# Kernel tuning notes

Measured on AMD Instinct MI355X. Metric: run time of the kernel, lower is better.

Reference implementation:

```python
import jax, jax.numpy as jnp
import numpy as np

H = 512
NHALF = 32  # N // 2 complex conjugate pairs
LLEN = 8192


def setup_inputs() -> dict:
    key = jax.random.key(0)
    k1, k2, k3 = jax.random.split(key, 3)
    # log_dt ~ uniform in [log(dt_min), log(dt_max)]
    log_dt = jax.random.uniform(k1, (H,), dtype=jnp.float32) * (
        np.log(0.1) - np.log(0.001)) + np.log(0.001)
    # C: complex randn stored as (H, NHALF, 2) real view
    C = jax.random.normal(k2, (H, NHALF, 2), dtype=jnp.float32)
    log_A_real = jnp.log(0.5 * jnp.ones((H, NHALF), dtype=jnp.float32))
    A_imag = np.pi * jnp.broadcast_to(
        jnp.arange(NHALF, dtype=jnp.float32), (H, NHALF))
    return {"C": C, "log_dt": log_dt, "log_A_real": log_A_real,
            "A_imag": A_imag, "L": LLEN}


def reference(C, log_dt, log_A_real, A_imag, L):
    # zoh discretization of diagonal SSM -> kernel K of shape (H, L)
    dt = jnp.exp(log_dt)                                  # (H,)
    Cc = (C[..., 0] + 1j * C[..., 1]).astype(jnp.complex64)  # (H, n)
    A = (-jnp.exp(log_A_real) + 1j * A_imag).astype(jnp.complex64)  # (H, n)
    dtA = A * dt[:, None]                                 # (H, n)
    t = jnp.arange(L, dtype=jnp.float32)                  # (L,)
    C_scaled = Cc * (jnp.exp(dtA) - 1.0) / A              # (H, n)
    # Vandermonde: exp(dtA)^t over length L, reduce over n
    T = jnp.exp(dtA[:, :, None] * t[None, None, :])       # (H, n, L) complex
    K = 2.0 * jnp.einsum('hn,hnl->hl', C_scaled, T).real  # (H, L)
    return K
```

## Files before the change

kernel.cpp:

```cpp
#include <hip/hip_runtime.h>
#include <math.h>

#define HDIM  512
#define NH    32
#define LLEN  8192
#define BLOCK 256
#define CHUNK (LLEN / BLOCK)

__global__ __launch_bounds__(BLOCK) void s4d_kernel(
    const float* __restrict__ C,
    const float* __restrict__ log_dt,
    const float* __restrict__ log_A_real,
    const float* __restrict__ A_imag,
    float* __restrict__ out)
{
    __shared__ float  s_cre[NH], s_cim[NH];
    __shared__ float  s_wre[NH], s_wim[NH];
    __shared__ float  s_dre[NH];
    __shared__ double s_dim[NH];

    const int h   = blockIdx.x;
    const int tid = threadIdx.x;

    if (tid < NH) {
        const int n = tid;
        const double TWO_PI = 6.283185307179586476925287;
        const double dt  = exp((double)log_dt[h]);
        const double Are = -exp((double)log_A_real[h * NH + n]);
        const double Aim = (double)A_imag[h * NH + n];
        const double dre = Are * dt, dim = Aim * dt;

        double es, ec;
        sincos(dim, &es, &ec);
        const double em   = exp(dre);
        const double nre  = em * ec - 1.0, nim = em * es;
        const double den  = Are * Are + Aim * Aim;
        const double fre  = (nre * Are + nim * Aim) / den;
        const double fim  = (nim * Are - nre * Aim) / den;
        const double Cre  = (double)C[(h * NH + n) * 2 + 0];
        const double Cim  = (double)C[(h * NH + n) * 2 + 1];
        s_cre[n] = (float)(2.0 * (Cre * fre - Cim * fim));
        s_cim[n] = (float)(2.0 * (Cre * fim + Cim * fre));

        double r = dim * (double)BLOCK * (1.0 / TWO_PI);
        r -= floor(r);
        double ss, cc;
        sincos(r * TWO_PI, &ss, &cc);
        const double m = exp(dre * (double)BLOCK);
        s_wre[n] = (float)(m * cc);
        s_wim[n] = (float)(m * ss);
        s_dre[n] = (float)dre;
        s_dim[n] = dim;
    }
    __syncthreads();

    float acc[CHUNK];
#pragma unroll
    for (int j = 0; j < CHUNK; ++j) acc[j] = 0.0f;

    const float ftid = (float)tid;
#pragma unroll 1
    for (int n = 0; n < NH; ++n) {
        const float cr = s_cre[n], ci = s_cim[n];
        const float wr = s_wre[n], wi = s_wim[n];

        const double TWO_PI = 6.283185307179586476925287;
        double r = s_dim[n] * (double)tid * (1.0 / TWO_PI);
        r -= floor(r);
        float s, c;
        __sincosf((float)(r * TWO_PI), &s, &c);
        const float mag = __expf(s_dre[n] * ftid);
        float Tr = mag * c, Ti = mag * s;

#pragma unroll
        for (int j = 0; j < CHUNK; ++j) {
            acc[j] = fmaf(cr, Tr, fmaf(-ci, Ti, acc[j]));
            const float nTr = fmaf(Tr, wr, -Ti * wi);
            const float nTi = fmaf(Tr, wi,  Ti * wr);
            Tr = nTr; Ti = nTi;
        }
    }

    float* orow = out + (size_t)h * LLEN + tid;
#pragma unroll
    for (int j = 0; j < CHUNK; ++j) orow[j * BLOCK] = acc[j];
}

extern "C" void kernel_launch(void* const* d_in, const int* in_sizes, int n_in,
                              void* d_out, int out_size, void* d_ws, size_t ws_size,
                              hipStream_t stream) {
    const float* C          = (const float*)d_in[0];
    const float* log_dt     = (const float*)d_in[1];
    const float* log_A_real = (const float*)d_in[2];
    const float* A_imag     = (const float*)d_in[3];
    float* out = (float*)d_out;

    s4d_kernel<<<HDIM, BLOCK, 0, stream>>>(C, log_dt, log_A_real, A_imag, out);
}
```

Measured before the change: 88.33 us.

## Split L across two blocks per head and store float4 runs per thread

The grid becomes 2 blocks per head, each covering half of L, so 1024 blocks are launched instead of 512 and more of the GPU is occupied. Each thread now owns 4 consecutive positions per step: it builds them from a seed using the single-step rotation w1, then advances all four by a 1024-step rotation. This enables float4 vectorized stores. The cost is that the per-n setup (double-precision range reduction, sincos, exp) runs in twice as many blocks, and the length-3 recurrence chain adds a little float error.

```diff
diff --git a/kernel.cpp b/kernel.cpp
--- a/kernel.cpp
+++ b/kernel.cpp
@@ -1,11 +1,13 @@
 #include <hip/hip_runtime.h>
 #include <math.h>
 
-#define HDIM  512
-#define NH    32
-#define LLEN  8192
-#define BLOCK 256
-#define CHUNK (LLEN / BLOCK)
+#define HDIM   512
+#define NH     32
+#define LLEN   8192
+#define BLOCK  256
+#define LSPLIT 2
+#define LPB    (LLEN / LSPLIT)
+#define JSTEPS (LPB / (BLOCK * 4))
 
 __global__ __launch_bounds__(BLOCK) void s4d_kernel(
     const float* __restrict__ C,
@@ -15,11 +17,13 @@
     float* __restrict__ out)
 {
     __shared__ float  s_cre[NH], s_cim[NH];
-    __shared__ float  s_wre[NH], s_wim[NH];
+    __shared__ float  s_w1r[NH], s_w1i[NH];
+    __shared__ float  s_Wr[NH],  s_Wi[NH];
     __shared__ float  s_dre[NH];
     __shared__ double s_dim[NH];
 
-    const int h   = blockIdx.x;
+    const int h   = blockIdx.y;
+    const int ls  = blockIdx.x;
     const int tid = threadIdx.x;
 
     if (tid < NH) {
@@ -32,58 +36,85 @@
 
         double es, ec;
         sincos(dim, &es, &ec);
-        const double em   = exp(dre);
-        const double nre  = em * ec - 1.0, nim = em * es;
-        const double den  = Are * Are + Aim * Aim;
-        const double fre  = (nre * Are + nim * Aim) / den;
-        const double fim  = (nim * Are - nre * Aim) / den;
-        const double Cre  = (double)C[(h * NH + n) * 2 + 0];
-        const double Cim  = (double)C[(h * NH + n) * 2 + 1];
+        const double em  = exp(dre);
+        const double nre = em * ec - 1.0, nim = em * es;
+        const double den = Are * Are + Aim * Aim;
+        const double fre = (nre * Are + nim * Aim) / den;
+        const double fim = (nim * Are - nre * Aim) / den;
+        const double Cre = (double)C[(h * NH + n) * 2 + 0];
+        const double Cim = (double)C[(h * NH + n) * 2 + 1];
         s_cre[n] = (float)(2.0 * (Cre * fre - Cim * fim));
         s_cim[n] = (float)(2.0 * (Cre * fim + Cim * fre));
 
-        double r = dim * (double)BLOCK * (1.0 / TWO_PI);
+        s_w1r[n] = (float)(em * ec);
+        s_w1i[n] = (float)(em * es);
+
+        double r = dim * 1024.0 * (1.0 / TWO_PI);
         r -= floor(r);
         double ss, cc;
         sincos(r * TWO_PI, &ss, &cc);
-        const double m = exp(dre * (double)BLOCK);
-        s_wre[n] = (float)(m * cc);
-        s_wim[n] = (float)(m * ss);
+        const double m = exp(dre * 1024.0);
+        s_Wr[n] = (float)(m * cc);
+        s_Wi[n] = (float)(m * ss);
+
         s_dre[n] = (float)dre;
         s_dim[n] = dim;
     }
     __syncthreads();
 
-    float acc[CHUNK];
+    const int lbase = ls * LPB + 4 * tid;
+    const float flbase = (float)lbase;
+
+    float acc[JSTEPS][4];
 #pragma unroll
-    for (int j = 0; j < CHUNK; ++j) acc[j] = 0.0f;
+    for (int j = 0; j < JSTEPS; ++j)
+#pragma unroll
+        for (int k = 0; k < 4; ++k) acc[j][k] = 0.0f;
 
-    const float ftid = (float)tid;
 #pragma unroll 1
     for (int n = 0; n < NH; ++n) {
         const float cr = s_cre[n], ci = s_cim[n];
-        const float wr = s_wre[n], wi = s_wim[n];
+        const float w1r = s_w1r[n], w1i = s_w1i[n];
+        const float Wr = s_Wr[n],  Wi = s_Wi[n];
 
         const double TWO_PI = 6.283185307179586476925287;
-        double r = s_dim[n] * (double)tid * (1.0 / TWO_PI);
+        double r = s_dim[n] * (double)lbase * (1.0 / TWO_PI);
         r -= floor(r);
         float s, c;
         __sincosf((float)(r * TWO_PI), &s, &c);
-        const float mag = __expf(s_dre[n] * ftid);
-        float Tr = mag * c, Ti = mag * s;
+        const float mag = __expf(s_dre[n] * flbase);
+
+        float Tr[4], Ti[4];
+        Tr[0] = mag * c;
+        Ti[0] = mag * s;
+#pragma unroll
+        for (int k = 1; k < 4; ++k) {
+            Tr[k] = fmaf(Tr[k-1], w1r, -Ti[k-1] * w1i);
+            Ti[k] = fmaf(Tr[k-1], w1i,  Ti[k-1] * w1r);
+        }
 
 #pragma unroll
-        for (int j = 0; j < CHUNK; ++j) {
-            acc[j] = fmaf(cr, Tr, fmaf(-ci, Ti, acc[j]));
-            const float nTr = fmaf(Tr, wr, -Ti * wi);
-            const float nTi = fmaf(Tr, wi,  Ti * wr);
-            Tr = nTr; Ti = nTi;
+        for (int j = 0; j < JSTEPS; ++j) {
+#pragma unroll
+            for (int k = 0; k < 4; ++k)
+                acc[j][k] = fmaf(cr, Tr[k], fmaf(-ci, Ti[k], acc[j][k]));
+            if (j < JSTEPS - 1) {
+#pragma unroll
+                for (int k = 0; k < 4; ++k) {
+                    const float nTr = fmaf(Tr[k], Wr, -Ti[k] * Wi);
+                    const float nTi = fmaf(Tr[k], Wi,  Ti[k] * Wr);
+                    Tr[k] = nTr; Ti[k] = nTi;
+                }
+            }
         }
     }
 
-    float* orow = out + (size_t)h * LLEN + tid;
+    float* orow = out + (size_t)h * LLEN;
 #pragma unroll
-    for (int j = 0; j < CHUNK; ++j) orow[j * BLOCK] = acc[j];
+    for (int j = 0; j < JSTEPS; ++j) {
+        float4 v = make_float4(acc[j][0], acc[j][1], acc[j][2], acc[j][3]);
+        *(float4*)(orow + lbase + j * (BLOCK * 4)) = v;
+    }
 }
 
 extern "C" void kernel_launch(void* const* d_in, const int* in_sizes, int n_in,
@@ -95,5 +126,6 @@
     const float* A_imag     = (const float*)d_in[3];
     float* out = (float*)d_out;
 
-    s4d_kernel<<<HDIM, BLOCK, 0, stream>>>(C, log_dt, log_A_real, A_imag, out);
+    dim3 grid(LSPLIT, HDIM);
+    s4d_kernel<<<grid, BLOCK, 0, stream>>>(C, log_dt, log_A_real, A_imag, out);
 }
```

After: 84.38 us. -4.5%, faster.

## Factor Vandermonde powers via two-level twiddle tables and float2 paired updates

Applied to the files above, without the earlier changes.

Replaces the per-thread double-precision range reduction and sincos/exp for each mode with shared-memory tables of w^(32*i) and w^(512*j), computed cooperatively by all threads in double precision. Each thread now owns 32 contiguous outputs, builds its starting power from one table product, and steps with w, w^4 and w^16 using paired float2 math that may map to packed FP32 instructions. Output stores become contiguous float4 writes per thread. Next-iteration shared loads are prefetched in registers. The cost is more setup work and shared memory, plus changed rounding from the chained multiplications.

```diff
diff --git a/kernel.cpp b/kernel.cpp
--- a/kernel.cpp
+++ b/kernel.cpp
@@ -5,7 +5,6 @@
 #define NH    32
 #define LLEN  8192
 #define BLOCK 256
-#define CHUNK (LLEN / BLOCK)
 
 __global__ __launch_bounds__(BLOCK) void s4d_kernel(
     const float* __restrict__ C,
@@ -14,76 +13,129 @@
     const float* __restrict__ A_imag,
     float* __restrict__ out)
 {
-    __shared__ float  s_cre[NH], s_cim[NH];
-    __shared__ float  s_wre[NH], s_wim[NH];
-    __shared__ float  s_dre[NH];
-    __shared__ double s_dim[NH];
+    __shared__ float2 tabA[NH + 1][16];
+    __shared__ float2 tabB[NH + 1][16];
+    __shared__ float4 s_c0[NH + 1];
+    __shared__ float4 s_c1[NH + 1];
 
     const int h   = blockIdx.x;
     const int tid = threadIdx.x;
 
-    if (tid < NH) {
-        const int n = tid;
-        const double TWO_PI = 6.283185307179586476925287;
+    {
+        const int n = tid & 31;
+        const int g = tid >> 5;
         const double dt  = exp((double)log_dt[h]);
         const double Are = -exp((double)log_A_real[h * NH + n]);
         const double Aim = (double)A_imag[h * NH + n];
         const double dre = Are * dt, dim = Aim * dt;
 
-        double es, ec;
-        sincos(dim, &es, &ec);
-        const double em   = exp(dre);
-        const double nre  = em * ec - 1.0, nim = em * es;
-        const double den  = Are * Are + Aim * Aim;
-        const double fre  = (nre * Are + nim * Aim) / den;
-        const double fim  = (nim * Are - nre * Aim) / den;
-        const double Cre  = (double)C[(h * NH + n) * 2 + 0];
-        const double Cim  = (double)C[(h * NH + n) * 2 + 1];
-        s_cre[n] = (float)(2.0 * (Cre * fre - Cim * fim));
-        s_cim[n] = (float)(2.0 * (Cre * fim + Cim * fre));
+        const bool   isB   = (g >= 4);
+        const double scale = isB ? 512.0 : 32.0;
+        const int    i0    = (isB ? (g - 4) : g) * 4;
 
-        double r = dim * (double)BLOCK * (1.0 / TWO_PI);
-        r -= floor(r);
-        double ss, cc;
-        sincos(r * TWO_PI, &ss, &cc);
-        const double m = exp(dre * (double)BLOCK);
-        s_wre[n] = (float)(m * cc);
-        s_wim[n] = (float)(m * ss);
-        s_dre[n] = (float)dre;
-        s_dim[n] = dim;
+        double s0, c0d; sincos(dim * scale * (double)i0, &s0, &c0d);
+        const double m0 = exp(dre * scale * (double)i0);
+        double er = m0 * c0d, ei = m0 * s0;
+        double ss, cs; sincos(dim * scale, &ss, &cs);
+        const double ms = exp(dre * scale);
+        const double str = ms * cs, sti = ms * ss;
+
+        float2* dst = isB ? &tabB[n][0] : &tabA[n][0];
+        for (int k = 0; k < 4; ++k) {
+            dst[i0 + k] = make_float2((float)er, (float)ei);
+            const double t = er * str - ei * sti;
+            ei = er * sti + ei * str;
+            er = t;
+        }
+
+        if (g == 0) {
+            double s1, c1; sincos(dim, &s1, &c1);
+            const double em  = exp(dre);
+            const double w1r = em * c1, w1i = em * s1;
+            const double nre = w1r - 1.0, nim = w1i;
+            const double den = Are * Are + Aim * Aim;
+            const double fre = (nre * Are + nim * Aim) / den;
+            const double fim = (nim * Are - nre * Aim) / den;
+            const double Cre = (double)C[(h * NH + n) * 2 + 0];
+            const double Cim = (double)C[(h * NH + n) * 2 + 1];
+            s_c0[n] = make_float4((float)(2.0 * (Cre * fre - Cim * fim)),
+                                  (float)(2.0 * (Cre * fim + Cim * fre)),
+                                  (float)w1r, (float)w1i);
+            double s4, c4;   sincos(dim * 4.0,  &s4,  &c4);
+            double s16, c16; sincos(dim * 16.0, &s16, &c16);
+            const double m4 = exp(dre * 4.0), m16 = exp(dre * 16.0);
+            s_c1[n] = make_float4((float)(m4 * c4),  (float)(m4 * s4),
+                                  (float)(m16 * c16), (float)(m16 * s16));
+        }
     }
     __syncthreads();
 
-    float acc[CHUNK];
+    const int lo = tid & 15, hi = tid >> 4;
+
+    float2 acc[4][4];
 #pragma unroll
-    for (int j = 0; j < CHUNK; ++j) acc[j] = 0.0f;
+    for (int j = 0; j < 4; ++j)
+#pragma unroll
+        for (int o = 0; o < 4; ++o) acc[j][o] = make_float2(0.f, 0.f);
 
-    const float ftid = (float)tid;
+    float2 A2 = tabA[0][lo], B2 = tabB[0][hi];
+    float4 k0 = s_c0[0],     k1 = s_c1[0];
+
 #pragma unroll 1
     for (int n = 0; n < NH; ++n) {
-        const float cr = s_cre[n], ci = s_cim[n];
-        const float wr = s_wre[n], wi = s_wim[n];
+        const float2 pA = tabA[n + 1][lo], pB = tabB[n + 1][hi];
+        const float4 p0 = s_c0[n + 1],     p1 = s_c1[n + 1];
 
-        const double TWO_PI = 6.283185307179586476925287;
-        double r = s_dim[n] * (double)tid * (1.0 / TWO_PI);
-        r -= floor(r);
-        float s, c;
-        __sincosf((float)(r * TWO_PI), &s, &c);
-        const float mag = __expf(s_dre[n] * ftid);
-        float Tr = mag * c, Ti = mag * s;
+        const float cr  = k0.x, ci  = k0.y, w1r = k0.z, w1i = k0.w;
+        const float W4r = k1.x, W4i = k1.y, W16r = k1.z, W16i = k1.w;
+
+        float Tr[4], Ti[4];
+        Tr[0] = fmaf(A2.x, B2.x, -(A2.y * B2.y));
+        Ti[0] = fmaf(A2.x, B2.y,  (A2.y * B2.x));
+#pragma unroll
+        for (int o = 1; o < 4; ++o) {
+            Tr[o] = fmaf(Tr[o-1], w1r, -(Ti[o-1] * w1i));
+            Ti[o] = fmaf(Tr[o-1], w1i,  (Ti[o-1] * w1r));
+        }
+        float2 Tr2[4], Ti2[4];
+#pragma unroll
+        for (int o = 0; o < 4; ++o) {
+            const float ur = fmaf(Tr[o], W16r, -(Ti[o] * W16i));
+            const float ui = fmaf(Tr[o], W16i,  (Ti[o] * W16r));
+            Tr2[o] = make_float2(Tr[o], ur);
+            Ti2[o] = make_float2(Ti[o], ui);
+        }
 
 #pragma unroll
-        for (int j = 0; j < CHUNK; ++j) {
-            acc[j] = fmaf(cr, Tr, fmaf(-ci, Ti, acc[j]));
-            const float nTr = fmaf(Tr, wr, -Ti * wi);
-            const float nTi = fmaf(Tr, wi,  Ti * wr);
-            Tr = nTr; Ti = nTi;
+        for (int j = 0; j < 4; ++j) {
+#pragma unroll
+            for (int o = 0; o < 4; ++o) {
+                acc[j][o].x = fmaf(cr, Tr2[o].x, fmaf(-ci, Ti2[o].x, acc[j][o].x));
+                acc[j][o].y = fmaf(cr, Tr2[o].y, fmaf(-ci, Ti2[o].y, acc[j][o].y));
+            }
+            if (j < 3) {
+#pragma unroll
+                for (int o = 0; o < 4; ++o) {
+                    const float nrx = fmaf(Tr2[o].x, W4r, -(Ti2[o].x * W4i));
+                    const float nry = fmaf(Tr2[o].y, W4r, -(Ti2[o].y * W4i));
+                    const float nix = fmaf(Tr2[o].x, W4i,  (Ti2[o].x * W4r));
+                    const float niy = fmaf(Tr2[o].y, W4i,  (Ti2[o].y * W4r));
+                    Tr2[o] = make_float2(nrx, nry);
+                    Ti2[o] = make_float2(nix, niy);
+                }
+            }
         }
+        A2 = pA; B2 = pB; k0 = p0; k1 = p1;
     }
 
-    float* orow = out + (size_t)h * LLEN + tid;
+    float* orow = out + (size_t)h * LLEN + 32 * tid;
 #pragma unroll
-    for (int j = 0; j < CHUNK; ++j) orow[j * BLOCK] = acc[j];
+    for (int j = 0; j < 4; ++j) {
+        *(float4*)(orow + 4 * j) =
+            make_float4(acc[j][0].x, acc[j][1].x, acc[j][2].x, acc[j][3].x);
+        *(float4*)(orow + 16 + 4 * j) =
+            make_float4(acc[j][0].y, acc[j][1].y, acc[j][2].y, acc[j][3].y);
+    }
 }
 
 extern "C" void kernel_launch(void* const* d_in, const int* in_sizes, int n_in,
```

New measurement: 84.51 us. -4.3%, faster.
